# Optimization experiments

Measured on AMD Instinct MI355X. Metric: run time of the kernel, lower is better.

Reference implementation:

```python
import jax, jax.numpy as jnp
import numpy as np

NEG_INF = -1e30  # stand-in for float('-inf'); avoids NaNs if a row is fully masked


def setup_inputs() -> dict:
    key = jax.random.key(0)
    k1, k2, k3, k4 = jax.random.split(key, 4)
    B, Q, K, D = 16, 2048, 2048, 64
    query = jax.random.normal(k1, (B, Q, D), dtype=jnp.float32)
    key_t = jax.random.normal(k2, (B, K, D), dtype=jnp.float32)
    value = jax.random.normal(k3, (B, K, D), dtype=jnp.float32)
    mask = jax.random.randint(k4, (B, Q, K), 0, 2).astype(jnp.bool_)
    return {"query": query, "key": key_t, "value": value, "mask": mask}


def reference(query, key, value, mask):
    d = query.shape[-1]
    # [B,Q,K] score matrix (naive attention, as in the original module)
    score = jnp.einsum('bqd,bkd->bqk', query, key) / jnp.sqrt(jnp.asarray(d, query.dtype))
    score = jnp.where(mask, NEG_INF, score)  # masked_fill(mask, -inf)
    attn = jax.nn.softmax(score, axis=-1)
    # dropout p=0.0 -> identity
    return jnp.einsum('bqk,bkd->bqd', attn, value)
```

## Files before the change

### kernel.cpp

```cpp
#include <hip/hip_runtime.h>


#define Bn   16
#define Qn   2048
#define Kseq 2048
#define Dn   64
#define QBLK 128
#define NEGF (-1e30f)

typedef __attribute__((ext_vector_type(4)))  short short4v;
typedef __attribute__((ext_vector_type(8)))  short short8;
typedef __attribute__((ext_vector_type(4)))  unsigned uint4v;
typedef __attribute__((ext_vector_type(16))) float f32x16;

static __device__ __forceinline__ short f2bf(float x) {
  union { float f; unsigned u; } un; un.f = x;
  unsigned r = un.u + 0x7FFFu + ((un.u >> 16) & 1u);
  return (short)(r >> 16);
}
static __device__ __forceinline__ unsigned pkbf(float lo, float hi) {
  unsigned r;
  asm("v_cvt_pk_bf16_f32 %0, %1, %2" : "=v"(r) : "v"(lo), "v"(hi));
  return r;
}
#if __has_builtin(__builtin_amdgcn_exp2f)
#define EXP2 __builtin_amdgcn_exp2f
#else
#define EXP2 exp2f
#endif
#define MFMA32 __builtin_amdgcn_mfma_f32_32x32x16_bf16

#define PREF_KV()                                                             \
  do {                                                                        \
    kst[0] = kp4[co0]; kst[1] = kp4[co1];                                     \
    kst[2] = kp4[co2]; kst[3] = kp4[co3];                                     \
    _Pragma("unroll")                                                         \
    for (int j2 = 0; j2 < 8; ++j2) vst[j2] = *(const float2*)(vp + j2 * 64);  \
    kp4 += 2048; vp += 8192;                                                  \
  } while (0)

#define PREF_M()                                                              \
  do {                                                                        \
    _Pragma("unroll")                                                         \
    for (int p = 0; p < 2; ++p)                                               \
      _Pragma("unroll")                                                       \
      for (int jj = 0; jj < 4; ++jj)                                          \
        mld[p * 4 + jj] = mpp[p * 32768 + jj];                                \
    mpp += 32;                                                                \
  } while (0)

#define WRITELDS()                                                            \
  do {                                                                        \
    _Pragma("unroll")                                                         \
    for (int i = 0; i < 4; ++i) {                                             \
      float4 a = kst[i]; short4v t;                                           \
      t[0] = f2bf(a.x); t[1] = f2bf(a.y); t[2] = f2bf(a.z); t[3] = f2bf(a.w); \
      *(short4v*)kdst[i] = t;                                                 \
    }                                                                         \
    short8 v0, v1;                                                            \
    _Pragma("unroll")                                                         \
    for (int j2 = 0; j2 < 8; ++j2) { v0[j2] = f2bf(vst[j2].x); v1[j2] = f2bf(vst[j2].y); } \
    *(short8*)vdst0 = v0; *(short8*)vdst1 = v1;                               \
    _Pragma("unroll")                                                         \
    for (int p = 0; p < 2; ++p) {                                             \
      unsigned v = 0;                                                         \
      _Pragma("unroll")                                                       \
      for (int jj = 0; jj < 4; ++jj) {                                        \
        int4 m = mld[p * 4 + jj];                                             \
        v |= (m.x != 0 ? 1u : 0u) << (jj * 4);                                \
        v |= (m.y != 0 ? 2u : 0u) << (jj * 4);                                \
        v |= (m.z != 0 ? 4u : 0u) << (jj * 4);                                \
        v |= (m.w != 0 ? 8u : 0u) << (jj * 4);                                \
      }                                                                       \
      mwr[p * 512] = (unsigned short)v;                                       \
    }                                                                         \
  } while (0)

#define COMPUTE()                                                             \
  do {                                                                        \
    const uint2 mb = *(const uint2*)mrd;                                      \
    const unsigned xh = mb.x >> (4 * h);                                      \
    const unsigned yh = mb.y >> (4 * h);                                      \
    f32x16 st0, st1;                                                          \
    _Pragma("unroll")                                                         \
    for (int i = 0; i < 16; ++i) { st0[i] = 0.f; st1[i] = 0.f; }              \
    _Pragma("unroll")                                                         \
    for (int s = 0; s < 4; ++s) {                                             \
      short8 kf = *(const short8*)(krd + ((32 * s + hh) ^ swz));              \
      st0 = MFMA32(kf, qf[s], st0, 0, 0, 0);                                  \
      short8 kg = *(const short8*)(krd + 4096 + ((32 * s + hh) ^ swz));       \
      st1 = MFMA32(kg, qf[s], st1, 0, 0, 0);                                  \
    }                                                                         \
    _Pragma("unroll")                                                         \
    for (int i = 0; i < 16; ++i) {                                            \
      const int bi = 8 * (i >> 2) + (i & 3);                                  \
      st0[i] = ((xh >> bi) & 1u) ? NEGF : st0[i];                             \
      st1[i] = ((yh >> bi) & 1u) ? NEGF : st1[i];                             \
    }                                                                         \
    float mx8[8];                                                             \
    _Pragma("unroll")                                                         \
    for (int i = 0; i < 8; ++i)                                               \
      mx8[i] = fmaxf(fmaxf(st0[i], st0[i+8]), fmaxf(st1[i], st1[i+8]));       \
    float mx = fmaxf(fmaxf(fmaxf(mx8[0],mx8[1]), fmaxf(mx8[2],mx8[3])),       \
                     fmaxf(fmaxf(mx8[4],mx8[5]), fmaxf(mx8[6],mx8[7])));      \
    mx = fmaxf(mx, __shfl_xor(mx, 32));                                       \
    if (!__all(mx <= mrun)) {                                                 \
      float mnew  = fmaxf(mrun, mx);                                          \
      float alpha = EXP2(mrun - mnew);                                        \
      lrun *= alpha;                                                          \
      _Pragma("unroll")                                                       \
      for (int i = 0; i < 16; ++i) { ot0[i] *= alpha; ot1[i] *= alpha; }      \
      mrun = mnew;                                                            \
    }                                                                         \
    _Pragma("unroll")                                                         \
    for (int i = 0; i < 16; ++i) {                                            \
      st0[i] = EXP2(st0[i] - mrun);                                           \
      st1[i] = EXP2(st1[i] - mrun);                                           \
    }                                                                         \
    float s8[8];                                                              \
    _Pragma("unroll")                                                         \
    for (int i = 0; i < 8; ++i) s8[i] = (st0[i]+st0[i+8]) + (st1[i]+st1[i+8]);\
    float lsum = ((s8[0]+s8[1]) + (s8[2]+s8[3])) +                            \
                 ((s8[4]+s8[5]) + (s8[6]+s8[7]));                             \
    lsum += __shfl_xor(lsum, 32);                                             \
    lrun += lsum;                                                             \
    short8 f0, f1, f2, f3;                                                    \
    {                                                                         \
      unsigned x0 = pkbf(st0[0],st0[1]),   x1 = pkbf(st0[2],st0[3]);          \
      unsigned y0 = pkbf(st0[4],st0[5]),   y1 = pkbf(st0[6],st0[7]);          \
      unsigned a0 = pkbf(st0[8],st0[9]),   a1 = pkbf(st0[10],st0[11]);        \
      unsigned b0 = pkbf(st0[12],st0[13]), b1 = pkbf(st0[14],st0[15]);        \
      unsigned sx0 = __shfl_xor(x0,32), sx1 = __shfl_xor(x1,32);              \
      unsigned sy0 = __shfl_xor(y0,32), sy1 = __shfl_xor(y1,32);              \
      unsigned sa0 = __shfl_xor(a0,32), sa1 = __shfl_xor(a1,32);              \
      unsigned sb0 = __shfl_xor(b0,32), sb1 = __shfl_xor(b1,32);              \
      uint4v u0 = { h ? sy0 : x0, h ? sy1 : x1, h ? y0 : sx0, h ? y1 : sx1 }; \
      uint4v u1 = { h ? sb0 : a0, h ? sb1 : a1, h ? b0 : sa0, h ? b1 : sa1 }; \
      f0 = __builtin_bit_cast(short8, u0);                                    \
      f1 = __builtin_bit_cast(short8, u1);                                    \
    }                                                                         \
    {                                                                         \
      unsigned x0 = pkbf(st1[0],st1[1]),   x1 = pkbf(st1[2],st1[3]);          \
      unsigned y0 = pkbf(st1[4],st1[5]),   y1 = pkbf(st1[6],st1[7]);          \
      unsigned a0 = pkbf(st1[8],st1[9]),   a1 = pkbf(st1[10],st1[11]);        \
      unsigned b0 = pkbf(st1[12],st1[13]), b1 = pkbf(st1[14],st1[15]);        \
      unsigned sx0 = __shfl_xor(x0,32), sx1 = __shfl_xor(x1,32);              \
      unsigned sy0 = __shfl_xor(y0,32), sy1 = __shfl_xor(y1,32);              \
      unsigned sa0 = __shfl_xor(a0,32), sa1 = __shfl_xor(a1,32);              \
      unsigned sb0 = __shfl_xor(b0,32), sb1 = __shfl_xor(b1,32);              \
      uint4v u2 = { h ? sy0 : x0, h ? sy1 : x1, h ? y0 : sx0, h ? y1 : sx1 }; \
      uint4v u3 = { h ? sb0 : a0, h ? sb1 : a1, h ? b0 : sa0, h ? b1 : sa1 }; \
      f2 = __builtin_bit_cast(short8, u2);                                    \
      f3 = __builtin_bit_cast(short8, u3);                                    \
    }                                                                         \
    _Pragma("unroll")                                                         \
    for (int s = 0; s < 4; ++s) {                                             \
      short8 pf = (s==0) ? f0 : (s==1) ? f1 : (s==2) ? f2 : f3;               \
      short8 va = *(const short8*)(vrd + ((32 * s + hh) ^ swz));              \
      ot0 = MFMA32(va, pf, ot0, 0, 0, 0);                                     \
      short8 vb = *(const short8*)(vrd + 4096 + ((32 * s + hh) ^ swz));       \
      ot1 = MFMA32(vb, pf, ot1, 0, 0, 0);                                     \
    }                                                                         \
  } while (0)

__launch_bounds__(512, 2)
__global__ void attn_fused(const float* __restrict__ Qg,
                           const float* __restrict__ Kg,
                           const float* __restrict__ Vg,
                           const int*   __restrict__ Mg,
                           float* __restrict__ Og) {
  __shared__ char ldsb[34816];

  const int tid  = threadIdx.x;
  const int lane = tid & 63;
  const int w    = tid >> 6;
  const int wq   = w & 3;
  const int grp  = w >> 2;
  const int l31  = lane & 31;
  const int h    = lane >> 5;
  const int hh   = h << 4;
  const int swz  = (l31 & 7) << 4;
  const int b    = blockIdx.y;
  const int qb   = blockIdx.x * QBLK;
  const int q    = qb + wq * 32 + l31;

  const float qscale = 0.18033688011112042f;
  const float* qp = Qg + ((size_t)(b * Qn + q)) * Dn + 8 * h;
  short8 qf[4];
#pragma unroll
  for (int s = 0; s < 4; ++s) {
    float4 a = *(const float4*)(qp + 16 * s);
    float4 c = *(const float4*)(qp + 16 * s + 4);
    short8 f;
    f[0]=f2bf(a.x*qscale); f[1]=f2bf(a.y*qscale); f[2]=f2bf(a.z*qscale); f[3]=f2bf(a.w*qscale);
    f[4]=f2bf(c.x*qscale); f[5]=f2bf(c.y*qscale); f[6]=f2bf(c.z*qscale); f[7]=f2bf(c.w*qscale);
    qf[s] = f;
  }

  const float4* kp4 = (const float4*)(Kg + (size_t)b * Kseq * Dn);
  const int co0 = tid, co1 = tid + 512, co2 = tid + 1024, co3 = tid + 1536;
  char* kdst[4];
#pragma unroll
  for (int i = 0; i < 4; ++i) {
    int c = tid + 512 * i;
    int row = c >> 4, col16 = c & 15;
    int tile = row >> 6, r = row & 63;
    kdst[i] = ldsb + tile * 8192 + r * 128 +
              (((col16 >> 1) << 4) ^ ((r & 7) << 4)) + ((col16 & 1) << 3);
  }

  const int uu = tid & 255, tileV = tid >> 8;
  const int d0 = (uu & 31) * 2, kv8 = (uu >> 5) * 8;
  const float* vp = Vg + ((size_t)b * Kseq + tileV * 64 + kv8) * Dn + d0;
  char* vdst0 = ldsb + 16384 + tileV * 8192 + d0 * 128 + ((kv8 * 2) ^ ((d0 & 7) << 4));
  char* vdst1 = ldsb + 16384 + tileV * 8192 + (d0 + 1) * 128 + ((kv8 * 2) ^ (((d0 + 1) & 7) << 4));

  const int4* mpp = (const int4*)(Mg + ((size_t)(b * Qn + qb + (tid >> 3))) * Kseq)
                    + (tid & 7) * 4;
  unsigned short* mwr = (unsigned short*)(ldsb + 32768) + (tid >> 3) * 8 + (tid & 7);
  const char* mrd = ldsb + 32768 + (wq * 32 + l31) * 16 + grp * 8;

  const char* krd = ldsb + grp * 8192 + l31 * 128;
  const char* vrd = ldsb + 16384 + grp * 8192 + l31 * 128;

  f32x16 ot0, ot1;
#pragma unroll
  for (int i = 0; i < 16; ++i) { ot0[i] = 0.f; ot1[i] = 0.f; }
  float mrun = NEGF, lrun = 0.f;

  float4 kst[4];
  float2 vst[8];
  int4   mld[8];

  PREF_KV();
  PREF_M();
  WRITELDS();
  __syncthreads();

#pragma unroll 1
  for (int j = 0; j < 16; ++j) {
    if (j < 15) { PREF_KV(); PREF_M(); }
    COMPUTE();
    if (j < 15) {
      __syncthreads();
      WRITELDS();
      __syncthreads();
    }
  }

  __syncthreads();

  float* lm = (float*)ldsb;
  float* ll = lm + 256;
  float* lo = ll + 256;
  const int s4 = wq * 64 + lane;
  if (grp == 1) {
    lm[s4] = mrun; ll[s4] = lrun;
#pragma unroll
    for (int i = 0; i < 16; ++i) lo[s4 * 20 + i] = ot0[i];
  }
  __syncthreads();
  float aA = 1.f, aB = 0.f;
  if (grp == 0) {
    float mB = lm[s4], lB = ll[s4];
    float ms = fmaxf(mrun, mB);
    aA = EXP2(mrun - ms); aB = EXP2(mB - ms);
    lrun = lrun * aA + lB * aB;
#pragma unroll
    for (int i = 0; i < 16; ++i) ot0[i] = ot0[i] * aA + lo[s4 * 20 + i] * aB;
  }
  __syncthreads();
  if (grp == 1) {
#pragma unroll
    for (int i = 0; i < 16; ++i) lo[s4 * 20 + i] = ot1[i];
  }
  __syncthreads();
  if (grp == 0) {
#pragma unroll
    for (int i = 0; i < 16; ++i) ot1[i] = ot1[i] * aA + lo[s4 * 20 + i] * aB;
    float inv = 1.0f / lrun;
    float* op = Og + ((size_t)(b * Qn + q)) * Dn;
#pragma unroll
    for (int g = 0; g < 4; ++g) {
      float4 o;
      o.x = ot0[4*g+0] * inv; o.y = ot0[4*g+1] * inv;
      o.z = ot0[4*g+2] * inv; o.w = ot0[4*g+3] * inv;
      *(float4*)(op + 8*g + 4*h) = o;
      o.x = ot1[4*g+0] * inv; o.y = ot1[4*g+1] * inv;
      o.z = ot1[4*g+2] * inv; o.w = ot1[4*g+3] * inv;
      *(float4*)(op + 32 + 8*g + 4*h) = o;
    }
  }
}

extern "C" void kernel_launch(void* const* d_in, const int* in_sizes, int n_in,
                              void* d_out, int out_size, void* d_ws, size_t ws_size,
                              hipStream_t stream) {
  const float* Q = (const float*)d_in[0];
  const float* K = (const float*)d_in[1];
  const float* V = (const float*)d_in[2];
  const int*   M = (const int*)d_in[3];
  float* O = (float*)d_out;
  dim3 grid(Qn / QBLK, Bn);
  attn_fused<<<grid, dim3(512), 0, stream>>>(Q, K, V, M, O);
}
```

Measured before the change: 380.4 us.

## Double-buffer K/V/mask LDS tiles and flatten grid with batch-fastest ordering

```diff
diff --git a/kernel.cpp b/kernel.cpp
--- a/kernel.cpp
+++ b/kernel.cpp
@@ -7,6 +7,7 @@
 #define Dn   64
 #define QBLK 128
 #define NEGF (-1e30f)
+#define BUF1 34816
 
 typedef __attribute__((ext_vector_type(4)))  short short4v;
 typedef __attribute__((ext_vector_type(8)))  short short8;
@@ -49,18 +50,18 @@
     mpp += 32;                                                                \
   } while (0)
 
-#define WRITELDS()                                                            \
+#define WRITELDS(OFF)                                                         \
   do {                                                                        \
     _Pragma("unroll")                                                         \
     for (int i = 0; i < 4; ++i) {                                             \
       float4 a = kst[i]; short4v t;                                           \
       t[0] = f2bf(a.x); t[1] = f2bf(a.y); t[2] = f2bf(a.z); t[3] = f2bf(a.w); \
-      *(short4v*)kdst[i] = t;                                                 \
+      *(short4v*)(kdst[i] + (OFF)) = t;                                       \
     }                                                                         \
     short8 v0, v1;                                                            \
     _Pragma("unroll")                                                         \
     for (int j2 = 0; j2 < 8; ++j2) { v0[j2] = f2bf(vst[j2].x); v1[j2] = f2bf(vst[j2].y); } \
-    *(short8*)vdst0 = v0; *(short8*)vdst1 = v1;                               \
+    *(short8*)(vdst0 + (OFF)) = v0; *(short8*)(vdst1 + (OFF)) = v1;           \
     _Pragma("unroll")                                                         \
     for (int p = 0; p < 2; ++p) {                                             \
       unsigned v = 0;                                                         \
@@ -72,13 +73,13 @@
         v |= (m.z != 0 ? 4u : 0u) << (jj * 4);                                \
         v |= (m.w != 0 ? 8u : 0u) << (jj * 4);                                \
       }                                                                       \
-      mwr[p * 512] = (unsigned short)v;                                       \
+      *(unsigned short*)(mwrb + (OFF) + p * 1024) = (unsigned short)v;        \
     }                                                                         \
   } while (0)
 
-#define COMPUTE()                                                             \
+#define COMPUTE(OFF)                                                          \
   do {                                                                        \
-    const uint2 mb = *(const uint2*)mrd;                                      \
+    const uint2 mb = *(const uint2*)(mrd + (OFF));                            \
     const unsigned xh = mb.x >> (4 * h);                                      \
     const unsigned yh = mb.y >> (4 * h);                                      \
     f32x16 st0, st1;                                                          \
@@ -86,9 +87,9 @@
     for (int i = 0; i < 16; ++i) { st0[i] = 0.f; st1[i] = 0.f; }              \
     _Pragma("unroll")                                                         \
     for (int s = 0; s < 4; ++s) {                                             \
-      short8 kf = *(const short8*)(krd + ((32 * s + hh) ^ swz));              \
+      short8 kf = *(const short8*)(krd + (OFF) + ((32 * s + hh) ^ swz));      \
       st0 = MFMA32(kf, qf[s], st0, 0, 0, 0);                                  \
-      short8 kg = *(const short8*)(krd + 4096 + ((32 * s + hh) ^ swz));       \
+      short8 kg = *(const short8*)(krd + (OFF) + 4096 + ((32 * s + hh) ^ swz));\
       st1 = MFMA32(kg, qf[s], st1, 0, 0, 0);                                  \
     }                                                                         \
     _Pragma("unroll")                                                         \
@@ -156,9 +157,9 @@
     _Pragma("unroll")                                                         \
     for (int s = 0; s < 4; ++s) {                                             \
       short8 pf = (s==0) ? f0 : (s==1) ? f1 : (s==2) ? f2 : f3;               \
-      short8 va = *(const short8*)(vrd + ((32 * s + hh) ^ swz));              \
+      short8 va = *(const short8*)(vrd + (OFF) + ((32 * s + hh) ^ swz));      \
       ot0 = MFMA32(va, pf, ot0, 0, 0, 0);                                     \
-      short8 vb = *(const short8*)(vrd + 4096 + ((32 * s + hh) ^ swz));       \
+      short8 vb = *(const short8*)(vrd + (OFF) + 4096 + ((32 * s + hh) ^ swz));\
       ot1 = MFMA32(vb, pf, ot1, 0, 0, 0);                                     \
     }                                                                         \
   } while (0)
@@ -169,7 +170,7 @@
                            const float* __restrict__ Vg,
                            const int*   __restrict__ Mg,
                            float* __restrict__ Og) {
-  __shared__ char ldsb[34816];
+  __shared__ char ldsb[2 * BUF1];
 
   const int tid  = threadIdx.x;
   const int lane = tid & 63;
@@ -180,8 +181,9 @@
   const int h    = lane >> 5;
   const int hh   = h << 4;
   const int swz  = (l31 & 7) << 4;
-  const int b    = blockIdx.y;
-  const int qb   = blockIdx.x * QBLK;
+  const int wgid = blockIdx.x;
+  const int b    = wgid & 15;
+  const int qb   = (wgid >> 4) * QBLK;
   const int q    = qb + wq * 32 + l31;
 
   const float qscale = 0.18033688011112042f;
@@ -217,7 +219,7 @@
 
   const int4* mpp = (const int4*)(Mg + ((size_t)(b * Qn + qb + (tid >> 3))) * Kseq)
                     + (tid & 7) * 4;
-  unsigned short* mwr = (unsigned short*)(ldsb + 32768) + (tid >> 3) * 8 + (tid & 7);
+  char* mwrb = ldsb + 32768 + ((tid >> 3) * 8 + (tid & 7)) * 2;
   const char* mrd = ldsb + 32768 + (wq * 32 + l31) * 16 + grp * 8;
 
   const char* krd = ldsb + grp * 8192 + l31 * 128;
@@ -232,23 +234,24 @@
   float2 vst[8];
   int4   mld[8];
 
-  PREF_KV();
-  PREF_M();
-  WRITELDS();
+  PREF_KV(); PREF_M();
+  WRITELDS(0);
+  PREF_KV(); PREF_M();
   __syncthreads();
 
 #pragma unroll 1
-  for (int j = 0; j < 16; ++j) {
-    if (j < 15) { PREF_KV(); PREF_M(); }
-    COMPUTE();
-    if (j < 15) {
-      __syncthreads();
-      WRITELDS();
+  for (int t = 0; t < 8; ++t) {
+    COMPUTE(0);
+    WRITELDS(BUF1);
+    if (t < 7) { PREF_KV(); PREF_M(); }
+    __syncthreads();
+    COMPUTE(BUF1);
+    if (t < 7) {
+      WRITELDS(0);
+      PREF_KV(); PREF_M();
       __syncthreads();
     }
   }
-
-  __syncthreads();
 
   float* lm = (float*)ldsb;
   float* ll = lm + 256;
@@ -301,6 +304,5 @@
   const float* V = (const float*)d_in[2];
   const int*   M = (const int*)d_in[3];
   float* O = (float*)d_out;
-  dim3 grid(Qn / QBLK, Bn);
-  attn_fused<<<grid, dim3(512), 0, stream>>>(Q, K, V, M, O);
+  attn_fused<<<dim3(256), dim3(512), 0, stream>>>(Q, K, V, M, O);
 }
```

Result: no change. 379.2 us (-0.3%).
